# Kernel optimization log

Measured on AMD Instinct MI355X. Metric: run time of the kernel, lower is better.

The kernel has to match this reference:

```python
import jax, jax.numpy as jnp
import numpy as np

PATCH = 16
LOSS_WEIGHT = 1.0


def setup_inputs() -> dict:
    key = jax.random.key(0)
    cls_score = jax.random.normal(key, (8, 19, 512, 512), dtype=jnp.float32)
    return {"cls_score": cls_score}


def reference(cls_score):
    # Faithful to NuclearLoss(patch_size=16, use_softmax=True, inverse=False,
    # reduction='mean').
    N, C, H, W = cls_score.shape
    p = PATCH
    ph, pw = H // p, W // p
    logits = jax.nn.softmax(cls_score, axis=1)  # softmax over channel dim
    # patchify: (N,C,H,W) -> (N*L, p*p, C) with L = ph*pw
    x = logits.reshape(N, C, ph, p, pw, p)
    x = jnp.einsum('nchpwq->nhwpqc', x)
    patches = x.reshape(N * ph * pw, p * p, C)  # (B, p^2, C)
    # Original: mats = sqrt(bmm(P^T, P)) elementwise, loss = -sum(trace(mat)).
    # Only the diagonal of P^T P is needed: diag_k = sum_i P[i,k]^2.
    diag = jnp.sum(patches * patches, axis=1)          # (B, C)
    loss = -jnp.sum(jnp.sqrt(diag))
    loss = loss / patches.shape[0]                      # reduction='mean'
    return LOSS_WEIGHT * loss
```

## Files before the change

kernel.cpp:

```cpp
#include <hip/hip_runtime.h>
#include <math.h>


#define CCH   19
#define WW    512
#define CHST  (512 * 512)
#define IMGST (CCH * CHST)

typedef float f4 __attribute__((ext_vector_type(4)));

__global__ __launch_bounds__(256, 2) void nuclear_patch_kernel(
    const float* __restrict__ in, float* __restrict__ out) {
    __shared__ float psum[4 * 16 * CCH];

    const int tid  = threadIdx.x;
    const int w    = tid >> 6;
    const int lane = tid & 63;
    const int b    = blockIdx.x;
    const int n    = b >> 6;
    const int rem  = b & 63;
    const int prow = rem >> 1;
    const int half = rem & 1;

    const float* base = in + (size_t)n * IMGST
                           + (size_t)(prow * 16 + w) * WW
                           + half * 256 + lane * 4;

    float part[CCH];
#pragma unroll
    for (int c = 0; c < CCH; ++c) part[c] = 0.0f;

#pragma unroll
    for (int i = 0; i < 4; ++i) {
        const f4* p = (const f4*)(base + (size_t)(i * 4) * WW);
        f4 e[CCH];
        f4 s = {0.0f, 0.0f, 0.0f, 0.0f};
#pragma unroll
        for (int c = 0; c < CCH; ++c) {
            f4 x = p[(size_t)c * (CHST / 4)];
            f4 ev;
            ev.x = __expf(x.x);
            ev.y = __expf(x.y);
            ev.z = __expf(x.z);
            ev.w = __expf(x.w);
            e[c] = ev;
            s += ev;
        }
        f4 inv;
        inv.x = 1.0f / s.x;
        inv.y = 1.0f / s.y;
        inv.z = 1.0f / s.z;
        inv.w = 1.0f / s.w;
#pragma unroll
        for (int c = 0; c < CCH; ++c) {
            const f4 t = e[c] * inv;
            part[c] += t.x * t.x + t.y * t.y + t.z * t.z + t.w * t.w;
        }
    }

#pragma unroll
    for (int c = 0; c < CCH; ++c) {
        float v = part[c];
        v += __shfl_down(v, 2, 4);
        v += __shfl_down(v, 1, 4);
        part[c] = v;
    }

    const int patch = lane >> 2;
    if ((lane & 3) == 0) {
#pragma unroll
        for (int c = 0; c < CCH; ++c)
            psum[(w * 16 + patch) * CCH + c] = part[c];
    }
    __syncthreads();

    float s = 0.0f;
    for (int k = tid; k < 16 * CCH; k += 256) {
        const float d = psum[k] + psum[304 + k] + psum[608 + k] + psum[912 + k];
        s += sqrtf(d);
    }
    s += __shfl_down(s, 32, 64);
    s += __shfl_down(s, 16, 64);
    s += __shfl_down(s, 8, 64);
    s += __shfl_down(s, 4, 64);
    s += __shfl_down(s, 2, 64);
    s += __shfl_down(s, 1, 64);

    __shared__ float wsum[4];
    if (lane == 0) wsum[w] = s;
    __syncthreads();
    if (tid == 0) {
        const float t = wsum[0] + wsum[1] + wsum[2] + wsum[3];
        atomicAdd(out, t * (-1.0f / 8192.0f));
    }
}

extern "C" void kernel_launch(void* const* d_in, const int* in_sizes, int n_in,
                              void* d_out, int out_size, void* d_ws, size_t ws_size,
                              hipStream_t stream) {
    const float* in = (const float*)d_in[0];
    float* out = (float*)d_out;
    hipMemsetAsync(out, 0, sizeof(float), stream);
    nuclear_patch_kernel<<<512, 256, 0, stream>>>(in, out);
}
```

Before: 242.5 us.

## Split patch loss into row-strip kernel plus workspace reduction kernel

```diff
diff --git a/kernel.cpp b/kernel.cpp
--- a/kernel.cpp
+++ b/kernel.cpp
@@ -7,89 +7,88 @@
 #define CHST  (512 * 512)
 #define IMGST (CCH * CHST)
 
-typedef float f4 __attribute__((ext_vector_type(4)));
+typedef float    f4 __attribute__((ext_vector_type(4)));
+typedef _Float16 h4 __attribute__((ext_vector_type(4)));
 
-__global__ __launch_bounds__(256, 2) void nuclear_patch_kernel(
-    const float* __restrict__ in, float* __restrict__ out) {
-    __shared__ float psum[4 * 16 * CCH];
+__global__ __launch_bounds__(256, 8) void nuclear_strip_kernel(
+    const float* __restrict__ in, float* __restrict__ ws) {
+    __shared__ float lds[4][16][CCH];
 
     const int tid  = threadIdx.x;
     const int w    = tid >> 6;
     const int lane = tid & 63;
     const int b    = blockIdx.x;
-    const int n    = b >> 6;
-    const int rem  = b & 63;
-    const int prow = rem >> 1;
-    const int half = rem & 1;
+    const int n    = b >> 8;
+    const int rp   = b & 255;
+    const int row  = rp * 2 + (w >> 1);
+    const int half = w & 1;
 
-    const float* base = in + (size_t)n * IMGST
-                           + (size_t)(prow * 16 + w) * WW
-                           + half * 256 + lane * 4;
+    const float* p = in + (size_t)n * IMGST + (size_t)row * WW
+                        + half * 256 + (lane << 2);
 
-    float part[CCH];
-#pragma unroll
-    for (int c = 0; c < CCH; ++c) part[c] = 0.0f;
-
-#pragma unroll
-    for (int i = 0; i < 4; ++i) {
-        const f4* p = (const f4*)(base + (size_t)(i * 4) * WW);
-        f4 e[CCH];
-        f4 s = {0.0f, 0.0f, 0.0f, 0.0f};
-#pragma unroll
-        for (int c = 0; c < CCH; ++c) {
-            f4 x = p[(size_t)c * (CHST / 4)];
-            f4 ev;
-            ev.x = __expf(x.x);
-            ev.y = __expf(x.y);
-            ev.z = __expf(x.z);
-            ev.w = __expf(x.w);
-            e[c] = ev;
-            s += ev;
-        }
-        f4 inv;
-        inv.x = 1.0f / s.x;
-        inv.y = 1.0f / s.y;
-        inv.z = 1.0f / s.z;
-        inv.w = 1.0f / s.w;
-#pragma unroll
-        for (int c = 0; c < CCH; ++c) {
-            const f4 t = e[c] * inv;
-            part[c] += t.x * t.x + t.y * t.y + t.z * t.z + t.w * t.w;
-        }
-    }
-
+    h4 h[CCH];
+    f4 s = {0.0f, 0.0f, 0.0f, 0.0f};
 #pragma unroll
     for (int c = 0; c < CCH; ++c) {
-        float v = part[c];
+        f4 x = *(const f4*)(p + (size_t)c * CHST);
+        f4 e;
+        e.x = __expf(x.x);
+        e.y = __expf(x.y);
+        e.z = __expf(x.z);
+        e.w = __expf(x.w);
+        s += e;
+        h[c] = __builtin_convertvector(e, h4);
+    }
+    f4 inv;
+    inv.x = 1.0f / s.x;
+    inv.y = 1.0f / s.y;
+    inv.z = 1.0f / s.z;
+    inv.w = 1.0f / s.w;
+
+    const int seg = lane >> 2;
+#pragma unroll
+    for (int c = 0; c < CCH; ++c) {
+        const f4 e = __builtin_convertvector(h[c], f4);
+        const f4 t = e * inv;
+        float v = t.x * t.x + t.y * t.y + t.z * t.z + t.w * t.w;
         v += __shfl_down(v, 2, 4);
         v += __shfl_down(v, 1, 4);
-        part[c] = v;
-    }
-
-    const int patch = lane >> 2;
-    if ((lane & 3) == 0) {
-#pragma unroll
-        for (int c = 0; c < CCH; ++c)
-            psum[(w * 16 + patch) * CCH + c] = part[c];
+        if ((lane & 3) == 0) lds[w][seg][c] = v;
     }
     __syncthreads();
 
-    float s = 0.0f;
-    for (int k = tid; k < 16 * CCH; k += 256) {
-        const float d = psum[k] + psum[304 + k] + psum[608 + k] + psum[912 + k];
-        s += sqrtf(d);
+    float* wsb = ws + (size_t)b * 608;
+    for (int k = tid; k < 608; k += 256) {
+        const int pc = k / CCH;
+        const int c  = k - pc * CCH;
+        const int hh = pc >> 4;
+        const int pp = pc & 15;
+        wsb[k] = lds[hh][pp][c] + lds[hh + 2][pp][c];
     }
-    s += __shfl_down(s, 32, 64);
-    s += __shfl_down(s, 16, 64);
-    s += __shfl_down(s, 8, 64);
-    s += __shfl_down(s, 4, 64);
-    s += __shfl_down(s, 2, 64);
-    s += __shfl_down(s, 1, 64);
+}
+
+__global__ __launch_bounds__(256) void nuclear_finish_kernel(
+    const float* __restrict__ ws, float* __restrict__ out) {
+    const int i = blockIdx.x * 256 + threadIdx.x;
+    const int g = i / 608;
+    const int s = i - g * 608;
+    const float* p = ws + (size_t)g * 8 * 608 + s;
+    float d = 0.0f;
+#pragma unroll
+    for (int j = 0; j < 8; ++j) d += p[j * 608];
+    float v = sqrtf(d);
+
+    v += __shfl_down(v, 32, 64);
+    v += __shfl_down(v, 16, 64);
+    v += __shfl_down(v, 8, 64);
+    v += __shfl_down(v, 4, 64);
+    v += __shfl_down(v, 2, 64);
+    v += __shfl_down(v, 1, 64);
 
     __shared__ float wsum[4];
-    if (lane == 0) wsum[w] = s;
+    if ((threadIdx.x & 63) == 0) wsum[threadIdx.x >> 6] = v;
     __syncthreads();
-    if (tid == 0) {
+    if (threadIdx.x == 0) {
         const float t = wsum[0] + wsum[1] + wsum[2] + wsum[3];
         atomicAdd(out, t * (-1.0f / 8192.0f));
     }
@@ -99,7 +98,11 @@
                               void* d_out, int out_size, void* d_ws, size_t ws_size,
                               hipStream_t stream) {
     const float* in = (const float*)d_in[0];
+    float* ws  = (float*)d_ws;
     float* out = (float*)d_out;
+
     hipMemsetAsync(out, 0, sizeof(float), stream);
-    nuclear_patch_kernel<<<512, 256, 0, stream>>>(in, out);
+
+    nuclear_strip_kernel<<<2048, 256, 0, stream>>>(in, ws);
+    nuclear_finish_kernel<<<608, 256, 0, stream>>>(ws, out);
 }
```

New measurement: 244.5 us. About the same (+0.8%).
